# Optimization experiments

Hardware: AMD Instinct MI355X
Metric: run time of the kernel (lower is better)

The kernel has to match this reference:

```python
import jax, jax.numpy as jnp
import numpy as np

DT = 0.01        # base_dt from __init__
DT_SCALE = 1.0   # forward default


def setup_inputs() -> dict:
    key = jax.random.key(0)
    k1, k2, k3, k4, k5 = jax.random.split(key, 5)
    B, D, R = 4096, 512, 128
    x = jax.random.normal(k1, (B, D), dtype=jnp.float32)
    v = jax.random.normal(k2, (B, D), dtype=jnp.float32)
    force = jax.random.normal(k3, (B, D), dtype=jnp.float32)
    U = jax.random.normal(k4, (D, R), dtype=jnp.float32) * (1.0 / np.sqrt(D))
    W = jax.random.normal(k5, (R, D), dtype=jnp.float32) * (1.0 / np.sqrt(R))
    return {"x": x, "v": v, "force": force, "U": U, "W": W, "steps": 8}


def reference(x, v, force, U, W, steps):
    dt = DT * DT_SCALE
    # Dormand-Prince (DP5) tableau
    a21 = 1/5
    a31, a32 = 3/40, 9/40
    a41, a42, a43 = 44/45, -56/15, 32/9
    a51, a52, a53, a54 = 19372/6561, -25360/2187, 64448/6561, -212/729
    a61, a62, a63, a64, a65 = 9017/3168, -355/33, 46732/5247, 49/176, -5103/18656
    b1, b3, b4, b5, b6 = 35/384, 500/1113, 125/192, -2187/6784, 11/84

    def dynamics(tx, tv):
        # low-rank Christoffel: gamma(v, x) = ((v @ U) * (x @ U)) @ W
        acc = -jnp.einsum('br,rd->bd', (tv @ U) * (tx @ U), W)
        return acc + force

    def step(carry, _):
        cx, cv = carry
        k1x = cv
        k1v = dynamics(cx, cv)
        x2 = cx + dt * (a21 * k1x); v2 = cv + dt * (a21 * k1v)
        k2x = v2; k2v = dynamics(x2, v2)
        x3 = cx + dt * (a31 * k1x + a32 * k2x)
        v3 = cv + dt * (a31 * k1v + a32 * k2v)
        k3x = v3; k3v = dynamics(x3, v3)
        x4 = cx + dt * (a41 * k1x + a42 * k2x + a43 * k3x)
        v4 = cv + dt * (a41 * k1v + a42 * k2v + a43 * k3v)
        k4x = v4; k4v = dynamics(x4, v4)
        x5 = cx + dt * (a51 * k1x + a52 * k2x + a53 * k3x + a54 * k4x)
        v5 = cv + dt * (a51 * k1v + a52 * k2v + a53 * k3v + a54 * k4v)
        k5x = v5; k5v = dynamics(x5, v5)
        x6 = cx + dt * (a61 * k1x + a62 * k2x + a63 * k3x + a64 * k4x + a65 * k5x)
        v6 = cv + dt * (a61 * k1v + a62 * k2v + a63 * k3v + a64 * k4v + a65 * k5v)
        k6x = v6; k6v = dynamics(x6, v6)
        nx = cx + dt * (b1 * k1x + b3 * k3x + b4 * k4x + b5 * k5x + b6 * k6x)
        nv = cv + dt * (b1 * k1v + b3 * k3v + b4 * k4v + b5 * k5v + b6 * k6v)
        return (nx, nv), None

    (fx, fv), _ = jax.lax.scan(step, (x, v), None, length=steps)
    return fx, fv
```

## Files before the change

kernel.cpp:

```cpp
#include <hip/hip_runtime.h>


typedef _Float16 v8h __attribute__((ext_vector_type(8)));
typedef float v4f __attribute__((ext_vector_type(4)));
typedef unsigned short u16;
typedef unsigned int u32;

#define MFMAH __builtin_amdgcn_mfma_f32_16x16x32_f16
#define INV2048 4.8828125e-4f
#define INV256  0.00390625f
#define SSTR 144

__device__ __forceinline__ float swap8(float x){
  return __int_as_float(
    __builtin_amdgcn_mov_dpp(__float_as_int(x), 0x128, 0xf, 0xf, true));
}

struct Tab {
  double a[7][7]; double b[7]; double A[7]; double XC[7][7]; double XF[7]; double cxc[7];
};
static constexpr Tab make_tab() {
  Tab t{};
  t.a[2][1]=1.0/5;
  t.a[3][1]=3.0/40;       t.a[3][2]=9.0/40;
  t.a[4][1]=44.0/45;      t.a[4][2]=-56.0/15;      t.a[4][3]=32.0/9;
  t.a[5][1]=19372.0/6561; t.a[5][2]=-25360.0/2187; t.a[5][3]=64448.0/6561; t.a[5][4]=-212.0/729;
  t.a[6][1]=9017.0/3168;  t.a[6][2]=-355.0/33;     t.a[6][3]=46732.0/5247; t.a[6][4]=49.0/176; t.a[6][5]=-5103.0/18656;
  t.b[1]=35.0/384; t.b[2]=0.0; t.b[3]=500.0/1113; t.b[4]=125.0/192; t.b[5]=-2187.0/6784; t.b[6]=11.0/84;
  for (int i=1;i<=6;++i){ double s=0; for(int j=1;j<i;++j) s+=t.a[i][j]; t.A[i]=s; }
  for (int i=1;i<=6;++i) for(int l=1;l<i;++l){ double s=0; for(int j=l+1;j<i;++j) s+=t.a[i][j]*t.a[j][l]; t.XC[i][l]=s; }
  for (int i=1;i<=6;++i){ double s=0; for(int j=1;j<i;++j) s+=t.a[i][j]*t.A[j]; t.XF[i]=s; }
  for (int j=1;j<=6;++j){ double s=0; for (int i=j+1;i<=6;++i) s+=t.b[i]*t.a[i][j]; t.cxc[j]=s; }
  return t;
}
static constexpr Tab TB = make_tab();

__device__ __forceinline__ int decode_steps(const void* p){
  int v = *(const int*)p;
  if (v >= 1 && v <= 512) return v;
  float f = *(const float*)p;
  if (f >= 1.f && f <= 512.f) return (int)f;
  return 8;
}
__device__ __forceinline__ void split2s(float x, _Float16& h, _Float16& l){
  h = (_Float16)x;
  l = (_Float16)((x - (float)h) * 2048.0f);
}

#define WS_GH 0
#define WS_GL 16384
#define WS_UH 32768
#define WS_UL 98304
#define WS_WH 163840
#define WS_WL 229376

__global__ __launch_bounds__(512) void k_prep(const float* __restrict__ Ug,
                                              const float* __restrict__ Wg,
                                              _Float16* __restrict__ ws){
  const int tid = threadIdx.x;
  if (blockIdx.x >= 8) {
    int t = (blockIdx.x - 8)*512 + tid;
    if (t < 65536) {
      int r = t >> 7, c = t & 127;
      _Float16 h, l; split2s(Ug[t]*256.f, h, l);
      int kb=r>>5, q2=(r>>3)&3, j=r&7, n2=c>>4, cl=c&15;
      int slot = ((n2*16+kb)*64 + q2*16+cl)*8 + j;
      ws[WS_UH + slot] = h; ws[WS_UL + slot] = l;
    } else {
      int idx = t - 65536;
      int r = idx >> 9, c = idx & 511;
      _Float16 h, l; split2s(Wg[idx]*256.f, h, l);
      int kb=r>>5, q2=(r>>3)&3, j=r&7, n2=c>>4, cl=c&15;
      int slot = ((n2*4+kb)*64 + q2*16+cl)*8 + j;
      ws[WS_WH + slot] = h; ws[WS_WL + slot] = l;
    }
  } else {
    const int b = blockIdx.x;
    const int ww = tid >> 6, lane = tid & 63, q = lane >> 4, c16 = lane & 15;
    const int nb = ww;
    v4f aH = {0,0,0,0}, aC0 = {0,0,0,0}, aC1 = {0,0,0,0};
    #pragma unroll
    for (int kb = 0; kb < 16; ++kb) {
      const float* wp = Wg + (b*16 + c16)*512 + kb*32 + q*8;
      float4 w0 = *(const float4*)wp;
      float4 w1 = *(const float4*)(wp + 4);
      float wv[8] = {w0.x,w0.y,w0.z,w0.w, w1.x,w1.y,w1.z,w1.w};
      v8h Ah, Al, Bh, Bl;
      #pragma unroll
      for (int j = 0; j < 8; ++j) {
        _Float16 h, l; split2s(-wv[j], h, l);
        Ah[j] = h; Al[j] = l;
        float uv = Ug[(kb*32 + q*8 + j)*128 + nb*16 + c16] * 256.f;
        split2s(uv, h, l);
        Bh[j] = h; Bl[j] = l;
      }
      aH = MFMAH(Ah, Bh, aH, 0,0,0);
      if (kb & 1) {
        aC1 = MFMAH(Ah, Bl, aC1, 0,0,0);
        aC1 = MFMAH(Al, Bh, aC1, 0,0,0);
      } else {
        aC0 = MFMAH(Ah, Bl, aC0, 0,0,0);
        aC0 = MFMAH(Al, Bh, aC0, 0,0,0);
      }
    }
    #pragma unroll
    for (int r = 0; r < 4; ++r) {
      float g = aH[r] + (aC0[r] + aC1[r])*INV2048;
      _Float16 h, l; split2s(g, h, l);
      int m = b*16 + 4*q + r, n = nb*16 + c16;
      int slot = (((n>>4)*4 + (m>>5))*64 + ((m>>3)&3)*16 + (n&15))*8 + (m&7);
      ws[WS_GH + slot] = h; ws[WS_GL + slot] = l;
    }
  }
}

#define ARENA 49920

__global__ __launch_bounds__(512,4) void dp5_main(
    const float* __restrict__ xg, const float* __restrict__ vg,
    const float* __restrict__ fg, const void* stepsp,
    const _Float16* __restrict__ ws, float* __restrict__ outg)
{
  __shared__ __align__(16) char arena[ARENA];
  _Float16* base = (_Float16*)arena;
  const _Float16* uH = ws + WS_UH;
  const _Float16* uL = ws + WS_UL;
  const _Float16* wH = ws + WS_WH;
  const _Float16* wL = ws + WS_WL;

  const int tid  = threadIdx.x;
  const int ww   = tid >> 6;
  const int lane = tid & 63;
  const int q    = lane >> 4;
  const int c16  = lane & 15;
  const int nb   = ww;
  const int kcol = nb*16 + c16;
  const int srcl = (q>>1)*16 + c16;
  const bool odd = (q & 1);
  const int rb   = blockIdx.x * 8;
  const int S    = decode_steps(stepsp);
  const float dt = 0.01f;
  const int  brow = c16 & 7;
  const bool hiC  = (c16 >= 8);
  const int  kc0  = nb*16 + 4*q + (hiC ? 2 : 0);

  v8h Gh[4], Gl[4];
  #pragma unroll
  for (int kb = 0; kb < 4; ++kb) {
    int off = ((nb*4 + kb)*64 + lane)*8;
    Gh[kb] = *(const v8h*)(ws + WS_GH + off);
    Gl[kb] = *(const v8h*)(ws + WS_GL + off);
  }

  _Float16* tH = base;
  _Float16* tL = base + 12480;
  const int r16 = tid >> 5, c0 = (tid & 31)*16;
  float xU0[2], vU0[2], fU0[2];
  {
    {
      const float* sp = (r16 < 8) ? (xg + (rb + r16)*512) : (vg + (rb + r16 - 8)*512);
      sp += c0;
      float4 g0 = *(const float4*)(sp);
      float4 g1 = *(const float4*)(sp + 4);
      float4 g2 = *(const float4*)(sp + 8);
      float4 g3 = *(const float4*)(sp + 12);
      float vals[16] = {g0.x,g0.y,g0.z,g0.w, g1.x,g1.y,g1.z,g1.w,
                        g2.x,g2.y,g2.z,g2.w, g3.x,g3.y,g3.z,g3.w};
      v8h vh0, vh1, vl0, vl1;
      #pragma unroll
      for (int j = 0; j < 8; ++j) {
        _Float16 h, l;
        split2s(vals[j], h, l);     vh0[j] = h; vl0[j] = l;
        split2s(vals[8+j], h, l);   vh1[j] = h; vl1[j] = l;
      }
      int o = r16*520 + c0;
      *(v8h*)(tH + o) = vh0; *(v8h*)(tH + o + 8) = vh1;
      *(v8h*)(tL + o) = vl0; *(v8h*)(tL + o + 8) = vl1;
    }
    if (r16 < 8) {
      const float* sp = fg + (rb + r16)*512 + c0;
      float4 g0 = *(const float4*)(sp);
      float4 g1 = *(const float4*)(sp + 4);
      float4 g2 = *(const float4*)(sp + 8);
      float4 g3 = *(const float4*)(sp + 12);
      float vals[16] = {g0.x,g0.y,g0.z,g0.w, g1.x,g1.y,g1.z,g1.w,
                        g2.x,g2.y,g2.z,g2.w, g3.x,g3.y,g3.z,g3.w};
      v8h vh0, vh1, vl0, vl1;
      #pragma unroll
      for (int j = 0; j < 8; ++j) {
        _Float16 h, l;
        split2s(vals[j], h, l);     vh0[j] = h; vl0[j] = l;
        split2s(vals[8+j], h, l);   vh1[j] = h; vl1[j] = l;
      }
      int o = (16 + r16)*520 + c0;
      *(v8h*)(tH + o) = vh0; *(v8h*)(tH + o + 8) = vh1;
      *(v8h*)(tL + o) = vl0; *(v8h*)(tL + o + 8) = vl1;
    }
    __syncthreads();

    v4f aH0={0,0,0,0}, aH1={0,0,0,0}, aC0={0,0,0,0}, aC1={0,0,0,0};
    v4f bH0={0,0,0,0}, bH1={0,0,0,0}, bC0={0,0,0,0}, bC1={0,0,0,0};
    const int arow1 = (c16 < 8) ? (16 + c16) : c16;
    #pragma unroll
    for (int kb = 0; kb < 16; ++kb) {
      int ao0 = c16*520 + kb*32 + q*8;
      int ao1 = arow1*520 + kb*32 + q*8;
      v8h Ah0 = *(const v8h*)(tH + ao0);
      v8h Al0 = *(const v8h*)(tL + ao0);
      v8h Ah1 = *(const v8h*)(tH + ao1);
      v8h Al1 = *(const v8h*)(tL + ao1);
      int bo = ((nb*16 + kb)*64 + lane)*8;
      v8h Bh = *(const v8h*)(uH + bo);
      v8h Bl = *(const v8h*)(uL + bo);
      if (kb & 1) {
        aH1 = MFMAH(Ah0, Bh, aH1, 0,0,0);
        aC1 = MFMAH(Ah0, Bl, aC1, 0,0,0);
        aC1 = MFMAH(Al0, Bh, aC1, 0,0,0);
        bH1 = MFMAH(Ah1, Bh, bH1, 0,0,0);
        bC1 = MFMAH(Ah1, Bl, bC1, 0,0,0);
        bC1 = MFMAH(Al1, Bh, bC1, 0,0,0);
      } else {
        aH0 = MFMAH(Ah0, Bh, aH0, 0,0,0);
        aC0 = MFMAH(Ah0, Bl, aC0, 0,0,0);
        aC0 = MFMAH(Al0, Bh, aC0, 0,0,0);
        bH0 = MFMAH(Ah1, Bh, bH0, 0,0,0);
        bC0 = MFMAH(Ah1, Bl, bC0, 0,0,0);
        bC0 = MFMAH(Al1, Bh, bC0, 0,0,0);
      }
    }
    float at0 = ((aH0[0]+aH1[0]) + (aC0[0]+aC1[0])*INV2048)*INV256;
    float at1 = ((aH0[1]+aH1[1]) + (aC0[1]+aC1[1])*INV2048)*INV256;
    float at2 = ((aH0[2]+aH1[2]) + (aC0[2]+aC1[2])*INV2048)*INV256;
    float at3 = ((aH0[3]+aH1[3]) + (aC0[3]+aC1[3])*INV2048)*INV256;
    float bt0 = ((bH0[0]+bH1[0]) + (bC0[0]+bC1[0])*INV2048)*INV256;
    float bt1 = ((bH0[1]+bH1[1]) + (bC0[1]+bC1[1])*INV2048)*INV256;
    float bt2 = ((bH0[2]+bH1[2]) + (bC0[2]+bC1[2])*INV2048)*INV256;
    float bt3 = ((bH0[3]+bH1[3]) + (bC0[3]+bC1[3])*INV2048)*INV256;
    {
      float sx0=__shfl(at0,srcl,64), sx1=__shfl(at1,srcl,64);
      float sx2=__shfl(at2,srcl,64), sx3=__shfl(at3,srcl,64);
      xU0[0] = odd ? sx2 : sx0; xU0[1] = odd ? sx3 : sx1;
      int srclv = srcl + 32;
      float sv0=__shfl(at0,srclv,64), sv1=__shfl(at1,srclv,64);
      float sv2=__shfl(at2,srclv,64), sv3=__shfl(at3,srclv,64);
      vU0[0] = odd ? sv2 : sv0; vU0[1] = odd ? sv3 : sv1;
    }
    {
      float sf0=__shfl(bt0,srcl,64), sf1=__shfl(bt1,srcl,64);
      float sf2=__shfl(bt2,srcl,64), sf3=__shfl(bt3,srcl,64);
      fU0[0] = odd ? sf2 : sf0; fU0[1] = odd ? sf3 : sf1;
    }
    __syncthreads();
  }

  float cxU2[2], cvU2[2], fU2[2];
  {
    float* T = (float*)arena;
    #pragma unroll
    for (int p2 = 0; p2 < 3; ++p2) {
      float i0 = (p2==0) ? xU0[0] : (p2==1) ? vU0[0] : fU0[0];
      float i1 = (p2==0) ? xU0[1] : (p2==1) ? vU0[1] : fU0[1];
      T[(2*q + 0)*132 + kcol] = i0;
      T[(2*q + 1)*132 + kcol] = i1;
      __syncthreads();
      float2 t2 = *(const float2*)(T + brow*132 + kc0);
      float* o = (p2==0) ? cxU2 : (p2==1) ? cvU2 : fU2;
      o[0] = t2.x; o[1] = t2.y;
      __syncthreads();
    }
  }

  float kU6[6][2], Rr2[2], QXa2[2];
  #pragma unroll
  for (int j = 0; j < 2; ++j) {
    Rr2[j] = 0.f; QXa2[j] = 0.f;
    #pragma unroll
    for (int l = 0; l < 6; ++l) kU6[l][j] = 0.f;
  }

  int pb = 0;
  for (int s = 0; s < S; ++s) {
    float accX[2], accV[2], Pbs[2], Pxcs[2];
    #pragma unroll
    for (int j = 0; j < 2; ++j) { accX[j]=0.f; accV[j]=0.f; Pbs[j]=0.f; Pxcs[j]=0.f; }

    #pragma unroll
    for (int i = 1; i <= 6; ++i) {
      _Float16* bT = base + (pb ? 2304 : 0);
      const float dtA   = dt*(float)TB.A[i];
      const float dt2XF = dt*dt*(float)TB.XF[i];
      const float bi    = (float)TB.b[i];
      const float ci    = (float)TB.cxc[i];
      {
        union { _Float16 h[2]; u32 u; } ph, pl;
        #pragma unroll
        for (int j2 = 0; j2 < 2; ++j2) {
          float vv = cvU2[j2] + dtA*fU2[j2];
          float xx = cxU2[j2] + dtA*cvU2[j2] + dt2XF*fU2[j2];
          #pragma unroll
          for (int l = 1; l < i; ++l) {
            vv += (dt*(float)TB.a[i][l]) * kU6[l-1][j2];
            xx += (dt*dt*(float)TB.XC[i][l]) * kU6[l-1][j2];
          }
          float p = vv*xx;
          Pbs[j2] += bi*p; Pxcs[j2] += ci*p;
          _Float16 h, l2; split2s(p, h, l2);
          ph.h[j2] = h; pl.h[j2] = l2;
        }
        *(u32*)(bT + brow*SSTR + kc0)       = ph.u;
        *(u32*)(bT + (8+brow)*SSTR + kc0)   = pl.u;
      }
      __syncthreads();
      const _Float16* bp = bT + c16*SSTR + q*8;
      v8h B0 = *(const v8h*)(bp);
      v8h B1 = *(const v8h*)(bp + 32);
      v8h B2 = *(const v8h*)(bp + 64);
      v8h B3 = *(const v8h*)(bp + 96);
      v4f C1 = {0,0,0,0}, C2 = {0,0,0,0};
      C1 = MFMAH(Gh[0], B0, C1, 0,0,0);  C2 = MFMAH(Gl[0], B0, C2, 0,0,0);
      C1 = MFMAH(Gh[1], B1, C1, 0,0,0);  C2 = MFMAH(Gl[1], B1, C2, 0,0,0);
      C1 = MFMAH(Gh[2], B2, C1, 0,0,0);  C2 = MFMAH(Gl[2], B2, C2, 0,0,0);
      C1 = MFMAH(Gh[3], B3, C1, 0,0,0);  C2 = MFMAH(Gl[3], B3, C2, 0,0,0);
      float kv[4];
      #pragma unroll
      for (int r = 0; r < 4; ++r) {
        float oth = swap8(C1[r]);
        kv[r] = (C1[r] + (oth + C2[r])*INV2048)*INV256;
      }
      float k2 = swap8(kv[2]);
      float k3 = swap8(kv[3]);
      float kva = hiC ? k2 : kv[0];
      float kvb = hiC ? k3 : kv[1];
      kU6[i-1][0] = kva; kU6[i-1][1] = kvb;
      accX[0] += ci*kva; accV[0] += bi*kva;
      accX[1] += ci*kvb; accV[1] += bi*kvb;
      pb ^= 1;
    }

    #pragma unroll
    for (int j = 0; j < 2; ++j) {
      float nx = cxU2[j] + dt*cvU2[j] + dt*dt*(accX[j] + 0.5f*fU2[j]);
      cvU2[j] += dt*(accV[j] + fU2[j]);
      cxU2[j]  = nx;
      QXa2[j] += Rr2[j] + Pxcs[j];
      Rr2[j]  += Pbs[j];
    }
  }

  __syncthreads();
  _Float16* RQh = base;
  _Float16* RQl = base + 2176;
  {
    union { _Float16 h[2]; u32 u; } t1, t2, t3, t4;
    #pragma unroll
    for (int j2 = 0; j2 < 2; ++j2) {
      _Float16 h, l;
      split2s(Rr2[j2], h, l);  t1.h[j2] = h; t2.h[j2] = l;
      split2s(QXa2[j2], h, l); t3.h[j2] = h; t4.h[j2] = l;
    }
    *(u32*)(RQh + brow*136 + kc0)     = t1.u;
    *(u32*)(RQl + brow*136 + kc0)     = t2.u;
    *(u32*)(RQh + (8+brow)*136 + kc0) = t3.u;
    *(u32*)(RQl + (8+brow)*136 + kc0) = t4.u;
  }
  __syncthreads();

  float* axs = (float*)(arena + 9216);
  float* abs_ = (float*)(arena + 25600);

  #pragma unroll
  for (int cbi = 0; cbi < 4; ++cbi) {
    int cb = nb*4 + cbi;
    v4f aH={0,0,0,0}, aC0={0,0,0,0}, aC1={0,0,0,0};
    #pragma unroll
    for (int kb = 0; kb < 4; ++kb) {
      int bo = ((cb*4 + kb)*64 + lane)*8;
      v8h Bh = *(const v8h*)(wH + bo);
      v8h Bl = *(const v8h*)(wL + bo);
      int ao = c16*136 + kb*32 + q*8;
      v8h Ah = *(const v8h*)(RQh + ao);
      v8h Al = *(const v8h*)(RQl + ao);
      aH = MFMAH(Ah, Bh, aH, 0,0,0);
      if (kb & 1) {
        aC1 = MFMAH(Ah, Bl, aC1, 0,0,0);
        aC1 = MFMAH(Al, Bh, aC1, 0,0,0);
      } else {
        aC0 = MFMAH(Ah, Bl, aC0, 0,0,0);
        aC0 = MFMAH(Al, Bh, aC0, 0,0,0);
      }
    }
    float r0 = (aH[0] + (aC0[0]+aC1[0])*INV2048)*INV256;
    float r1 = (aH[1] + (aC0[1]+aC1[1])*INV2048)*INV256;
    float r2 = (aH[2] + (aC0[2]+aC1[2])*INV2048)*INV256;
    float r3 = (aH[3] + (aC0[3]+aC1[3])*INV2048)*INV256;
    float o0 = __shfl_xor(r0, 32, 64);
    float o1 = __shfl_xor(r1, 32, 64);
    float o2 = __shfl_xor(r2, 32, 64);
    float o3 = __shfl_xor(r3, 32, 64);
    if (q < 2) {
      float abv[4] = {r0, r1, r2, r3};
      float axv[4] = {o0, o1, o2, o3};
      #pragma unroll
      for (int i4 = 0; i4 < 4; ++i4) {
        int lrow = 4*q + i4;
        int lcol = cb*16 + c16;
        axs[lrow*512 + lcol]  = axv[i4];
        abs_[lrow*512 + lcol] = abv[i4];
      }
    }
  }
  __syncthreads();

  const float Sdt = (float)S * dt;
  #pragma unroll
  for (int half = 0; half < 2; ++half) {
    int flat = half*2048 + tid*4;
    int row  = flat >> 9;
    int col  = flat & 511;
    int go   = (rb + row)*512 + col;
    float4 xv = *(const float4*)(xg + go);
    float4 vv = *(const float4*)(vg + go);
    float4 fv = *(const float4*)(fg + go);
    float4 axf = *(const float4*)(axs + flat);
    float4 abf = *(const float4*)(abs_ + flat);
    float4 o1, o2;
    o1.x = xv.x + Sdt*vv.x + 0.5f*Sdt*Sdt*fv.x - dt*dt*axf.x;
    o1.y = xv.y + Sdt*vv.y + 0.5f*Sdt*Sdt*fv.y - dt*dt*axf.y;
    o1.z = xv.z + Sdt*vv.z + 0.5f*Sdt*Sdt*fv.z - dt*dt*axf.z;
    o1.w = xv.w + Sdt*vv.w + 0.5f*Sdt*Sdt*fv.w - dt*dt*axf.w;
    o2.x = vv.x + Sdt*fv.x - dt*abf.x;
    o2.y = vv.y + Sdt*fv.y - dt*abf.y;
    o2.z = vv.z + Sdt*fv.z - dt*abf.z;
    o2.w = vv.w + Sdt*fv.w - dt*abf.w;
    *(float4*)(outg + go) = o1;
    *(float4*)(outg + 2097152 + go) = o2;
  }
}

extern "C" void kernel_launch(void* const* d_in, const int* in_sizes, int n_in,
                              void* d_out, int out_size, void* d_ws, size_t ws_size,
                              hipStream_t stream) {
  const float* x = (const float*)d_in[0];
  const float* v = (const float*)d_in[1];
  const float* f = (const float*)d_in[2];
  const float* U = (const float*)d_in[3];
  const float* W = (const float*)d_in[4];
  _Float16* ws = (_Float16*)d_ws;

  k_prep<<<dim3(264), dim3(512), 0, stream>>>(U, W, ws);
  dp5_main<<<dim3(512), dim3(512), 0, stream>>>(
      x, v, f, d_in[5], ws, (float*)d_out);
}
```

Baseline: 136.4 us.

## Precompute next-stage RK partial sums off critical path, trim post-MFMA swaps, stagger block start

Before each stage's barrier and MFMA, the code now precomputes the partial sums for the next stage's inputs from the already-known k values. Only the newest k term is added after the MFMA result arrives, which shortens the serial dependency chain between stages. The post-MFMA reduction is reordered so the DPP swaps run on raw accumulator values and the selects happen before the arithmetic, using fewer dependent swaps. It also adds an s_sleep for blocks with blockIdx bit 8 set, staggering their start, which can shift contention but also adds idle time.

```diff
diff --git a/kernel.cpp b/kernel.cpp
--- a/kernel.cpp
+++ b/kernel.cpp
@@ -127,6 +127,8 @@
   const _Float16* uL = ws + WS_UL;
   const _Float16* wH = ws + WS_WH;
   const _Float16* wL = ws + WS_WL;
+
+  if (blockIdx.x & 256) __builtin_amdgcn_s_sleep(19);
 
   const int tid  = threadIdx.x;
   const int ww   = tid >> 6;
@@ -284,23 +286,27 @@
     #pragma unroll
     for (int j = 0; j < 2; ++j) { accX[j]=0.f; accV[j]=0.f; Pbs[j]=0.f; Pxcs[j]=0.f; }
 
+    float vvP[2], xxP[2];
+    #pragma unroll
+    for (int j2 = 0; j2 < 2; ++j2) {
+      vvP[j2] = cvU2[j2] + (dt*(float)TB.A[1])*fU2[j2];
+      xxP[j2] = cxU2[j2] + (dt*(float)TB.A[1])*cvU2[j2] + (dt*dt*(float)TB.XF[1])*fU2[j2];
+    }
+
     #pragma unroll
     for (int i = 1; i <= 6; ++i) {
       _Float16* bT = base + (pb ? 2304 : 0);
-      const float dtA   = dt*(float)TB.A[i];
-      const float dt2XF = dt*dt*(float)TB.XF[i];
       const float bi    = (float)TB.b[i];
       const float ci    = (float)TB.cxc[i];
       {
         union { _Float16 h[2]; u32 u; } ph, pl;
         #pragma unroll
         for (int j2 = 0; j2 < 2; ++j2) {
-          float vv = cvU2[j2] + dtA*fU2[j2];
-          float xx = cxU2[j2] + dtA*cvU2[j2] + dt2XF*fU2[j2];
-          #pragma unroll
-          for (int l = 1; l < i; ++l) {
-            vv += (dt*(float)TB.a[i][l]) * kU6[l-1][j2];
-            xx += (dt*dt*(float)TB.XC[i][l]) * kU6[l-1][j2];
+          float vv = vvP[j2];
+          float xx = xxP[j2];
+          if (i >= 2) {
+            vv += (dt*(float)TB.a[i][i-1]) * kU6[i-2][j2];
+            xx += (dt*dt*(float)TB.XC[i][i-1]) * kU6[i-2][j2];
           }
           float p = vv*xx;
           Pbs[j2] += bi*p; Pxcs[j2] += ci*p;
@@ -309,6 +315,19 @@
         }
         *(u32*)(bT + brow*SSTR + kc0)       = ph.u;
         *(u32*)(bT + (8+brow)*SSTR + kc0)   = pl.u;
+      }
+      if (i < 6) {
+        #pragma unroll
+        for (int j2 = 0; j2 < 2; ++j2) {
+          float vv = cvU2[j2] + (dt*(float)TB.A[i+1])*fU2[j2];
+          float xx = cxU2[j2] + (dt*(float)TB.A[i+1])*cvU2[j2] + (dt*dt*(float)TB.XF[i+1])*fU2[j2];
+          #pragma unroll
+          for (int l = 1; l < i; ++l) {
+            vv += (dt*(float)TB.a[i+1][l]) * kU6[l-1][j2];
+            xx += (dt*dt*(float)TB.XC[i+1][l]) * kU6[l-1][j2];
+          }
+          vvP[j2] = vv; xxP[j2] = xx;
+        }
       }
       __syncthreads();
       const _Float16* bp = bT + c16*SSTR + q*8;
@@ -321,19 +340,21 @@
       C1 = MFMAH(Gh[1], B1, C1, 0,0,0);  C2 = MFMAH(Gl[1], B1, C2, 0,0,0);
       C1 = MFMAH(Gh[2], B2, C1, 0,0,0);  C2 = MFMAH(Gl[2], B2, C2, 0,0,0);
       C1 = MFMAH(Gh[3], B3, C1, 0,0,0);  C2 = MFMAH(Gl[3], B3, C2, 0,0,0);
-      float kv[4];
-      #pragma unroll
-      for (int r = 0; r < 4; ++r) {
-        float oth = swap8(C1[r]);
-        kv[r] = (C1[r] + (oth + C2[r])*INV2048)*INV256;
-      }
-      float k2 = swap8(kv[2]);
-      float k3 = swap8(kv[3]);
-      float kva = hiC ? k2 : kv[0];
-      float kvb = hiC ? k3 : kv[1];
-      kU6[i-1][0] = kva; kU6[i-1][1] = kvb;
-      accX[0] += ci*kva; accV[0] += bi*kva;
-      accX[1] += ci*kvb; accV[1] += bi*kvb;
+      {
+        float sa0 = swap8(C1[0]), sa2 = swap8(C1[2]), sc2 = swap8(C2[2]);
+        float sb1 = swap8(C1[1]), sb3 = swap8(C1[3]), sd3 = swap8(C2[3]);
+        float m_a = hiC ? sa2   : C1[0];
+        float n_a = hiC ? C1[2] : sa0;
+        float c_a = hiC ? sc2   : C2[0];
+        float m_b = hiC ? sb3   : C1[1];
+        float n_b = hiC ? C1[3] : sb1;
+        float c_b = hiC ? sd3   : C2[1];
+        float kva = (m_a + (n_a + c_a)*INV2048)*INV256;
+        float kvb = (m_b + (n_b + c_b)*INV2048)*INV256;
+        kU6[i-1][0] = kva; kU6[i-1][1] = kvb;
+        accX[0] += ci*kva; accV[0] += bi*kva;
+        accX[1] += ci*kvb; accV[1] += bi*kvb;
+      }
       pb ^= 1;
     }
 
```

After: 136.2 us (median of 2 runs). No clear change (-0.2%).

## Halve block size to 256 threads with two column groups per wave

Applied to the files above, without the earlier changes.

Restructures the main DP5 kernel to use 4 waves per block instead of 8, with each wave handling two 16-column groups of the rank dimension. Per-wave register state doubles (kU, accumulators, G fragments, MFMA accumulators) and the epilogue keeps the A operand fragments in registers across column blocks. The prologue now transposes all three projections with a single LDS round trip instead of three, and the upper half of the blocks issue an s_sleep at the start to stagger their launch. The aim is fewer threads per barrier and less redundant LDS traffic, at the cost of higher register pressure and less occupancy per block.

```diff
diff --git a/kernel.cpp b/kernel.cpp
--- a/kernel.cpp
+++ b/kernel.cpp
@@ -3,8 +3,8 @@
 
 typedef _Float16 v8h __attribute__((ext_vector_type(8)));
 typedef float v4f __attribute__((ext_vector_type(4)));
-typedef unsigned short u16;
 typedef unsigned int u32;
+typedef unsigned long long u64;
 
 #define MFMAH __builtin_amdgcn_mfma_f32_16x16x32_f16
 #define INV2048 4.8828125e-4f
@@ -116,7 +116,7 @@
 
 #define ARENA 49920
 
-__global__ __launch_bounds__(512,4) void dp5_main(
+__global__ __launch_bounds__(256,2) void dp5_main(
     const float* __restrict__ xg, const float* __restrict__ vg,
     const float* __restrict__ fg, const void* stepsp,
     const _Float16* __restrict__ ws, float* __restrict__ outg)
@@ -128,78 +128,66 @@
   const _Float16* wH = ws + WS_WH;
   const _Float16* wL = ws + WS_WL;
 
+  if (blockIdx.x & 256) __builtin_amdgcn_s_sleep(19);
+
   const int tid  = threadIdx.x;
-  const int ww   = tid >> 6;
+  const int w    = tid >> 6;
   const int lane = tid & 63;
   const int q    = lane >> 4;
   const int c16  = lane & 15;
-  const int nb   = ww;
-  const int kcol = nb*16 + c16;
-  const int srcl = (q>>1)*16 + c16;
-  const bool odd = (q & 1);
   const int rb   = blockIdx.x * 8;
   const int S    = decode_steps(stepsp);
   const float dt = 0.01f;
   const int  brow = c16 & 7;
   const bool hiC  = (c16 >= 8);
-  const int  kc0  = nb*16 + 4*q + (hiC ? 2 : 0);
-
-  v8h Gh[4], Gl[4];
-  #pragma unroll
-  for (int kb = 0; kb < 4; ++kb) {
-    int off = ((nb*4 + kb)*64 + lane)*8;
-    Gh[kb] = *(const v8h*)(ws + WS_GH + off);
-    Gl[kb] = *(const v8h*)(ws + WS_GL + off);
-  }
+  const int  kc0n = w*32 + (hiC ? 16 : 0) + 4*q;
 
   _Float16* tH = base;
   _Float16* tL = base + 12480;
-  const int r16 = tid >> 5, c0 = (tid & 31)*16;
-  float xU0[2], vU0[2], fU0[2];
   {
+    const int row = tid >> 4;
+    const int c0  = (tid & 15) * 32;
     {
-      const float* sp = (r16 < 8) ? (xg + (rb + r16)*512) : (vg + (rb + r16 - 8)*512);
+      const float* sp = (row < 8) ? (xg + (rb + row)*512) : (vg + (rb + row - 8)*512);
       sp += c0;
-      float4 g0 = *(const float4*)(sp);
-      float4 g1 = *(const float4*)(sp + 4);
-      float4 g2 = *(const float4*)(sp + 8);
-      float4 g3 = *(const float4*)(sp + 12);
-      float vals[16] = {g0.x,g0.y,g0.z,g0.w, g1.x,g1.y,g1.z,g1.w,
-                        g2.x,g2.y,g2.z,g2.w, g3.x,g3.y,g3.z,g3.w};
-      v8h vh0, vh1, vl0, vl1;
-      #pragma unroll
-      for (int j = 0; j < 8; ++j) {
-        _Float16 h, l;
-        split2s(vals[j], h, l);     vh0[j] = h; vl0[j] = l;
-        split2s(vals[8+j], h, l);   vh1[j] = h; vl1[j] = l;
-      }
-      int o = r16*520 + c0;
-      *(v8h*)(tH + o) = vh0; *(v8h*)(tH + o + 8) = vh1;
-      *(v8h*)(tL + o) = vl0; *(v8h*)(tL + o + 8) = vl1;
-    }
-    if (r16 < 8) {
-      const float* sp = fg + (rb + r16)*512 + c0;
-      float4 g0 = *(const float4*)(sp);
-      float4 g1 = *(const float4*)(sp + 4);
-      float4 g2 = *(const float4*)(sp + 8);
-      float4 g3 = *(const float4*)(sp + 12);
-      float vals[16] = {g0.x,g0.y,g0.z,g0.w, g1.x,g1.y,g1.z,g1.w,
-                        g2.x,g2.y,g2.z,g2.w, g3.x,g3.y,g3.z,g3.w};
-      v8h vh0, vh1, vl0, vl1;
-      #pragma unroll
-      for (int j = 0; j < 8; ++j) {
-        _Float16 h, l;
-        split2s(vals[j], h, l);     vh0[j] = h; vl0[j] = l;
-        split2s(vals[8+j], h, l);   vh1[j] = h; vl1[j] = l;
-      }
-      int o = (16 + r16)*520 + c0;
-      *(v8h*)(tH + o) = vh0; *(v8h*)(tH + o + 8) = vh1;
-      *(v8h*)(tL + o) = vl0; *(v8h*)(tL + o + 8) = vl1;
-    }
-    __syncthreads();
-
-    v4f aH0={0,0,0,0}, aH1={0,0,0,0}, aC0={0,0,0,0}, aC1={0,0,0,0};
-    v4f bH0={0,0,0,0}, bH1={0,0,0,0}, bC0={0,0,0,0}, bC1={0,0,0,0};
+      #pragma unroll
+      for (int b2 = 0; b2 < 4; ++b2) {
+        float4 g0 = *(const float4*)(sp + b2*8);
+        float4 g1 = *(const float4*)(sp + b2*8 + 4);
+        float vals[8] = {g0.x,g0.y,g0.z,g0.w, g1.x,g1.y,g1.z,g1.w};
+        v8h vh, vl;
+        #pragma unroll
+        for (int j = 0; j < 8; ++j) { _Float16 h,l; split2s(vals[j],h,l); vh[j]=h; vl[j]=l; }
+        int o = row*520 + c0 + b2*8;
+        *(v8h*)(tH + o) = vh; *(v8h*)(tL + o) = vl;
+      }
+    }
+    if (tid < 128) {
+      const int rowf = tid >> 4;
+      const float* sp = fg + (rb + rowf)*512 + c0;
+      #pragma unroll
+      for (int b2 = 0; b2 < 4; ++b2) {
+        float4 g0 = *(const float4*)(sp + b2*8);
+        float4 g1 = *(const float4*)(sp + b2*8 + 4);
+        float vals[8] = {g0.x,g0.y,g0.z,g0.w, g1.x,g1.y,g1.z,g1.w};
+        v8h vh, vl;
+        #pragma unroll
+        for (int j = 0; j < 8; ++j) { _Float16 h,l; split2s(vals[j],h,l); vh[j]=h; vl[j]=l; }
+        int o = (16 + rowf)*520 + c0 + b2*8;
+        *(v8h*)(tH + o) = vh; *(v8h*)(tL + o) = vl;
+      }
+    }
+  }
+  __syncthreads();
+
+  float cxU4[4], cvU4[4], fU4[4];
+  {
+    v4f AH0[2],AH1[2],AC0[2],AC1[2],BH0[2],BH1[2],BC0[2],BC1[2];
+    #pragma unroll
+    for (int g=0; g<2; ++g){
+      AH0[g]=v4f{0,0,0,0}; AH1[g]=v4f{0,0,0,0}; AC0[g]=v4f{0,0,0,0}; AC1[g]=v4f{0,0,0,0};
+      BH0[g]=v4f{0,0,0,0}; BH1[g]=v4f{0,0,0,0}; BC0[g]=v4f{0,0,0,0}; BC1[g]=v4f{0,0,0,0};
+    }
     const int arow1 = (c16 < 8) ? (16 + c16) : c16;
     #pragma unroll
     for (int kb = 0; kb < 16; ++kb) {
@@ -209,80 +197,85 @@
       v8h Al0 = *(const v8h*)(tL + ao0);
       v8h Ah1 = *(const v8h*)(tH + ao1);
       v8h Al1 = *(const v8h*)(tL + ao1);
-      int bo = ((nb*16 + kb)*64 + lane)*8;
-      v8h Bh = *(const v8h*)(uH + bo);
-      v8h Bl = *(const v8h*)(uL + bo);
-      if (kb & 1) {
-        aH1 = MFMAH(Ah0, Bh, aH1, 0,0,0);
-        aC1 = MFMAH(Ah0, Bl, aC1, 0,0,0);
-        aC1 = MFMAH(Al0, Bh, aC1, 0,0,0);
-        bH1 = MFMAH(Ah1, Bh, bH1, 0,0,0);
-        bC1 = MFMAH(Ah1, Bl, bC1, 0,0,0);
-        bC1 = MFMAH(Al1, Bh, bC1, 0,0,0);
+      #pragma unroll
+      for (int g = 0; g < 2; ++g) {
+        int bo = (((2*w+g)*16 + kb)*64 + lane)*8;
+        v8h Bh = *(const v8h*)(uH + bo);
+        v8h Bl = *(const v8h*)(uL + bo);
+        if (kb & 1) {
+          AH1[g] = MFMAH(Ah0, Bh, AH1[g], 0,0,0);
+          AC1[g] = MFMAH(Ah0, Bl, AC1[g], 0,0,0);
+          AC1[g] = MFMAH(Al0, Bh, AC1[g], 0,0,0);
+          BH1[g] = MFMAH(Ah1, Bh, BH1[g], 0,0,0);
+          BC1[g] = MFMAH(Ah1, Bl, BC1[g], 0,0,0);
+          BC1[g] = MFMAH(Al1, Bh, BC1[g], 0,0,0);
+        } else {
+          AH0[g] = MFMAH(Ah0, Bh, AH0[g], 0,0,0);
+          AC0[g] = MFMAH(Ah0, Bl, AC0[g], 0,0,0);
+          AC0[g] = MFMAH(Al0, Bh, AC0[g], 0,0,0);
+          BH0[g] = MFMAH(Ah1, Bh, BH0[g], 0,0,0);
+          BC0[g] = MFMAH(Ah1, Bl, BC0[g], 0,0,0);
+          BC0[g] = MFMAH(Al1, Bh, BC0[g], 0,0,0);
+        }
+      }
+    }
+    __syncthreads();
+    float* T = (float*)arena;
+    #pragma unroll
+    for (int g = 0; g < 2; ++g) {
+      float ar[4], br[4];
+      #pragma unroll
+      for (int r = 0; r < 4; ++r) {
+        ar[r] = ((AH0[g][r]+AH1[g][r]) + (AC0[g][r]+AC1[g][r])*INV2048)*INV256;
+        br[r] = ((BH0[g][r]+BH1[g][r]) + (BC0[g][r]+BC1[g][r])*INV2048)*INV256;
+      }
+      int colc = (2*w+g)*16 + c16;
+      if (q < 2) {
+        #pragma unroll
+        for (int r = 0; r < 4; ++r) {
+          T[(4*q+r)*132 + colc]        = ar[r];
+          T[2112 + (4*q+r)*132 + colc] = br[r];
+        }
       } else {
-        aH0 = MFMAH(Ah0, Bh, aH0, 0,0,0);
-        aC0 = MFMAH(Ah0, Bl, aC0, 0,0,0);
-        aC0 = MFMAH(Al0, Bh, aC0, 0,0,0);
-        bH0 = MFMAH(Ah1, Bh, bH0, 0,0,0);
-        bC0 = MFMAH(Ah1, Bl, bC0, 0,0,0);
-        bC0 = MFMAH(Al1, Bh, bC0, 0,0,0);
-      }
-    }
-    float at0 = ((aH0[0]+aH1[0]) + (aC0[0]+aC1[0])*INV2048)*INV256;
-    float at1 = ((aH0[1]+aH1[1]) + (aC0[1]+aC1[1])*INV2048)*INV256;
-    float at2 = ((aH0[2]+aH1[2]) + (aC0[2]+aC1[2])*INV2048)*INV256;
-    float at3 = ((aH0[3]+aH1[3]) + (aC0[3]+aC1[3])*INV2048)*INV256;
-    float bt0 = ((bH0[0]+bH1[0]) + (bC0[0]+bC1[0])*INV2048)*INV256;
-    float bt1 = ((bH0[1]+bH1[1]) + (bC0[1]+bC1[1])*INV2048)*INV256;
-    float bt2 = ((bH0[2]+bH1[2]) + (bC0[2]+bC1[2])*INV2048)*INV256;
-    float bt3 = ((bH0[3]+bH1[3]) + (bC0[3]+bC1[3])*INV2048)*INV256;
-    {
-      float sx0=__shfl(at0,srcl,64), sx1=__shfl(at1,srcl,64);
-      float sx2=__shfl(at2,srcl,64), sx3=__shfl(at3,srcl,64);
-      xU0[0] = odd ? sx2 : sx0; xU0[1] = odd ? sx3 : sx1;
-      int srclv = srcl + 32;
-      float sv0=__shfl(at0,srclv,64), sv1=__shfl(at1,srclv,64);
-      float sv2=__shfl(at2,srclv,64), sv3=__shfl(at3,srclv,64);
-      vU0[0] = odd ? sv2 : sv0; vU0[1] = odd ? sv3 : sv1;
-    }
-    {
-      float sf0=__shfl(bt0,srcl,64), sf1=__shfl(bt1,srcl,64);
-      float sf2=__shfl(bt2,srcl,64), sf3=__shfl(bt3,srcl,64);
-      fU0[0] = odd ? sf2 : sf0; fU0[1] = odd ? sf3 : sf1;
+        #pragma unroll
+        for (int r = 0; r < 4; ++r) {
+          T[1056 + (4*(q-2)+r)*132 + colc] = ar[r];
+        }
+      }
     }
     __syncthreads();
-  }
-
-  float cxU2[2], cvU2[2], fU2[2];
-  {
-    float* T = (float*)arena;
-    #pragma unroll
-    for (int p2 = 0; p2 < 3; ++p2) {
-      float i0 = (p2==0) ? xU0[0] : (p2==1) ? vU0[0] : fU0[0];
-      float i1 = (p2==0) ? xU0[1] : (p2==1) ? vU0[1] : fU0[1];
-      T[(2*q + 0)*132 + kcol] = i0;
-      T[(2*q + 1)*132 + kcol] = i1;
-      __syncthreads();
-      float2 t2 = *(const float2*)(T + brow*132 + kc0);
-      float* o = (p2==0) ? cxU2 : (p2==1) ? cvU2 : fU2;
-      o[0] = t2.x; o[1] = t2.y;
-      __syncthreads();
-    }
-  }
-
-  float kU6[6][2], Rr2[2], QXa2[2];
+    float4 tx = *(const float4*)(T +        brow*132 + kc0n);
+    float4 tv = *(const float4*)(T + 1056 + brow*132 + kc0n);
+    float4 tf = *(const float4*)(T + 2112 + brow*132 + kc0n);
+    cxU4[0]=tx.x; cxU4[1]=tx.y; cxU4[2]=tx.z; cxU4[3]=tx.w;
+    cvU4[0]=tv.x; cvU4[1]=tv.y; cvU4[2]=tv.z; cvU4[3]=tv.w;
+    fU4[0]=tf.x;  fU4[1]=tf.y;  fU4[2]=tf.z;  fU4[3]=tf.w;
+    __syncthreads();
+  }
+
+  v8h Gh[2][4], Gl[2][4];
   #pragma unroll
-  for (int j = 0; j < 2; ++j) {
-    Rr2[j] = 0.f; QXa2[j] = 0.f;
-    #pragma unroll
-    for (int l = 0; l < 6; ++l) kU6[l][j] = 0.f;
+  for (int g = 0; g < 2; ++g)
+    #pragma unroll
+    for (int kb = 0; kb < 4; ++kb) {
+      int off = (((2*w+g)*4 + kb)*64 + lane)*8;
+      Gh[g][kb] = *(const v8h*)(ws + WS_GH + off);
+      Gl[g][kb] = *(const v8h*)(ws + WS_GL + off);
+    }
+
+  float kU[6][4], Rr[4], QX[4];
+  #pragma unroll
+  for (int j = 0; j < 4; ++j) {
+    Rr[j] = 0.f; QX[j] = 0.f;
+    #pragma unroll
+    for (int l = 0; l < 6; ++l) kU[l][j] = 0.f;
   }
 
   int pb = 0;
   for (int s = 0; s < S; ++s) {
-    float accX[2], accV[2], Pbs[2], Pxcs[2];
-    #pragma unroll
-    for (int j = 0; j < 2; ++j) { accX[j]=0.f; accV[j]=0.f; Pbs[j]=0.f; Pxcs[j]=0.f; }
+    float accX[4], accV[4], Pb[4], Pxc[4];
+    #pragma unroll
+    for (int j = 0; j < 4; ++j) { accX[j]=0.f; accV[j]=0.f; Pb[j]=0.f; Pxc[j]=0.f; }
 
     #pragma unroll
     for (int i = 1; i <= 6; ++i) {
@@ -292,23 +285,23 @@
       const float bi    = (float)TB.b[i];
       const float ci    = (float)TB.cxc[i];
       {
-        union { _Float16 h[2]; u32 u; } ph, pl;
-        #pragma unroll
-        for (int j2 = 0; j2 < 2; ++j2) {
-          float vv = cvU2[j2] + dtA*fU2[j2];
-          float xx = cxU2[j2] + dtA*cvU2[j2] + dt2XF*fU2[j2];
+        union { _Float16 h[4]; u64 u; } ph, pl;
+        #pragma unroll
+        for (int j2 = 0; j2 < 4; ++j2) {
+          float vv = cvU4[j2] + dtA*fU4[j2];
+          float xx = cxU4[j2] + dtA*cvU4[j2] + dt2XF*fU4[j2];
           #pragma unroll
           for (int l = 1; l < i; ++l) {
-            vv += (dt*(float)TB.a[i][l]) * kU6[l-1][j2];
-            xx += (dt*dt*(float)TB.XC[i][l]) * kU6[l-1][j2];
+            vv += (dt*(float)TB.a[i][l]) * kU[l-1][j2];
+            xx += (dt*dt*(float)TB.XC[i][l]) * kU[l-1][j2];
           }
           float p = vv*xx;
-          Pbs[j2] += bi*p; Pxcs[j2] += ci*p;
+          Pb[j2] += bi*p; Pxc[j2] += ci*p;
           _Float16 h, l2; split2s(p, h, l2);
           ph.h[j2] = h; pl.h[j2] = l2;
         }
-        *(u32*)(bT + brow*SSTR + kc0)       = ph.u;
-        *(u32*)(bT + (8+brow)*SSTR + kc0)   = pl.u;
+        *(u64*)(bT + brow*SSTR + kc0n)     = ph.u;
+        *(u64*)(bT + (8+brow)*SSTR + kc0n) = pl.u;
       }
       __syncthreads();
       const _Float16* bp = bT + c16*SSTR + q*8;
@@ -316,34 +309,34 @@
       v8h B1 = *(const v8h*)(bp + 32);
       v8h B2 = *(const v8h*)(bp + 64);
       v8h B3 = *(const v8h*)(bp + 96);
-      v4f C1 = {0,0,0,0}, C2 = {0,0,0,0};
-      C1 = MFMAH(Gh[0], B0, C1, 0,0,0);  C2 = MFMAH(Gl[0], B0, C2, 0,0,0);
-      C1 = MFMAH(Gh[1], B1, C1, 0,0,0);  C2 = MFMAH(Gl[1], B1, C2, 0,0,0);
-      C1 = MFMAH(Gh[2], B2, C1, 0,0,0);  C2 = MFMAH(Gl[2], B2, C2, 0,0,0);
-      C1 = MFMAH(Gh[3], B3, C1, 0,0,0);  C2 = MFMAH(Gl[3], B3, C2, 0,0,0);
-      float kv[4];
+      v4f C1[2], C2[2];
+      #pragma unroll
+      for (int g = 0; g < 2; ++g) {
+        C1[g] = v4f{0,0,0,0}; C2[g] = v4f{0,0,0,0};
+        C1[g] = MFMAH(Gh[g][0], B0, C1[g], 0,0,0);  C2[g] = MFMAH(Gl[g][0], B0, C2[g], 0,0,0);
+        C1[g] = MFMAH(Gh[g][1], B1, C1[g], 0,0,0);  C2[g] = MFMAH(Gl[g][1], B1, C2[g], 0,0,0);
+        C1[g] = MFMAH(Gh[g][2], B2, C1[g], 0,0,0);  C2[g] = MFMAH(Gl[g][2], B2, C2[g], 0,0,0);
+        C1[g] = MFMAH(Gh[g][3], B3, C1[g], 0,0,0);  C2[g] = MFMAH(Gl[g][3], B3, C2[g], 0,0,0);
+      }
       #pragma unroll
       for (int r = 0; r < 4; ++r) {
-        float oth = swap8(C1[r]);
-        kv[r] = (C1[r] + (oth + C2[r])*INV2048)*INV256;
-      }
-      float k2 = swap8(kv[2]);
-      float k3 = swap8(kv[3]);
-      float kva = hiC ? k2 : kv[0];
-      float kvb = hiC ? k3 : kv[1];
-      kU6[i-1][0] = kva; kU6[i-1][1] = kvb;
-      accX[0] += ci*kva; accV[0] += bi*kva;
-      accX[1] += ci*kvb; accV[1] += bi*kvb;
+        float kv0 = (C1[0][r] + (swap8(C1[0][r]) + C2[0][r])*INV2048)*INV256;
+        float kv1 = (C1[1][r] + (swap8(C1[1][r]) + C2[1][r])*INV2048)*INV256;
+        float sk1 = swap8(kv1);
+        float kk  = hiC ? sk1 : kv0;
+        kU[i-1][r] = kk;
+        accX[r] += ci*kk; accV[r] += bi*kk;
+      }
       pb ^= 1;
     }
 
     #pragma unroll
-    for (int j = 0; j < 2; ++j) {
-      float nx = cxU2[j] + dt*cvU2[j] + dt*dt*(accX[j] + 0.5f*fU2[j]);
-      cvU2[j] += dt*(accV[j] + fU2[j]);
-      cxU2[j]  = nx;
-      QXa2[j] += Rr2[j] + Pxcs[j];
-      Rr2[j]  += Pbs[j];
+    for (int j = 0; j < 4; ++j) {
+      float nx = cxU4[j] + dt*cvU4[j] + dt*dt*(accX[j] + 0.5f*fU4[j]);
+      cvU4[j] += dt*(accV[j] + fU4[j]);
+      cxU4[j]  = nx;
+      QX[j] += Rr[j] + Pxc[j];
+      Rr[j] += Pb[j];
     }
   }
 
@@ -351,61 +344,69 @@
   _Float16* RQh = base;
   _Float16* RQl = base + 2176;
   {
-    union { _Float16 h[2]; u32 u; } t1, t2, t3, t4;
-    #pragma unroll
-    for (int j2 = 0; j2 < 2; ++j2) {
+    union { _Float16 h[4]; u64 u; } t1, t2, t3, t4;
+    #pragma unroll
+    for (int j2 = 0; j2 < 4; ++j2) {
       _Float16 h, l;
-      split2s(Rr2[j2], h, l);  t1.h[j2] = h; t2.h[j2] = l;
-      split2s(QXa2[j2], h, l); t3.h[j2] = h; t4.h[j2] = l;
-    }
-    *(u32*)(RQh + brow*136 + kc0)     = t1.u;
-    *(u32*)(RQl + brow*136 + kc0)     = t2.u;
-    *(u32*)(RQh + (8+brow)*136 + kc0) = t3.u;
-    *(u32*)(RQl + (8+brow)*136 + kc0) = t4.u;
+      split2s(Rr[j2], h, l);  t1.h[j2] = h; t2.h[j2] = l;
+      split2s(QX[j2], h, l);  t3.h[j2] = h; t4.h[j2] = l;
+    }
+    *(u64*)(RQh + brow*136 + kc0n)     = t1.u;
+    *(u64*)(RQl + brow*136 + kc0n)     = t2.u;
+    *(u64*)(RQh + (8+brow)*136 + kc0n) = t3.u;
+    *(u64*)(RQl + (8+brow)*136 + kc0n) = t4.u;
   }
   __syncthreads();
 
-  float* axs = (float*)(arena + 9216);
+  v8h EAh[4], EAl[4];
+  #pragma unroll
+  for (int kb = 0; kb < 4; ++kb) {
+    int ao = c16*136 + kb*32 + q*8;
+    EAh[kb] = *(const v8h*)(RQh + ao);
+    EAl[kb] = *(const v8h*)(RQl + ao);
+  }
+
+  float* axs  = (float*)(arena + 9216);
   float* abs_ = (float*)(arena + 25600);
 
   #pragma unroll
-  for (int cbi = 0; cbi < 4; ++cbi) {
-    int cb = nb*4 + cbi;
-    v4f aH={0,0,0,0}, aC0={0,0,0,0}, aC1={0,0,0,0};
-    #pragma unroll
-    for (int kb = 0; kb < 4; ++kb) {
-      int bo = ((cb*4 + kb)*64 + lane)*8;
-      v8h Bh = *(const v8h*)(wH + bo);
-      v8h Bl = *(const v8h*)(wL + bo);
-      int ao = c16*136 + kb*32 + q*8;
-      v8h Ah = *(const v8h*)(RQh + ao);
-      v8h Al = *(const v8h*)(RQl + ao);
-      aH = MFMAH(Ah, Bh, aH, 0,0,0);
-      if (kb & 1) {
-        aC1 = MFMAH(Ah, Bl, aC1, 0,0,0);
-        aC1 = MFMAH(Al, Bh, aC1, 0,0,0);
-      } else {
-        aC0 = MFMAH(Ah, Bl, aC0, 0,0,0);
-        aC0 = MFMAH(Al, Bh, aC0, 0,0,0);
-      }
-    }
-    float r0 = (aH[0] + (aC0[0]+aC1[0])*INV2048)*INV256;
-    float r1 = (aH[1] + (aC0[1]+aC1[1])*INV2048)*INV256;
-    float r2 = (aH[2] + (aC0[2]+aC1[2])*INV2048)*INV256;
-    float r3 = (aH[3] + (aC0[3]+aC1[3])*INV2048)*INV256;
-    float o0 = __shfl_xor(r0, 32, 64);
-    float o1 = __shfl_xor(r1, 32, 64);
-    float o2 = __shfl_xor(r2, 32, 64);
-    float o3 = __shfl_xor(r3, 32, 64);
-    if (q < 2) {
-      float abv[4] = {r0, r1, r2, r3};
-      float axv[4] = {o0, o1, o2, o3};
-      #pragma unroll
-      for (int i4 = 0; i4 < 4; ++i4) {
-        int lrow = 4*q + i4;
-        int lcol = cb*16 + c16;
-        axs[lrow*512 + lcol]  = axv[i4];
-        abs_[lrow*512 + lcol] = abv[i4];
+  for (int g = 0; g < 2; ++g) {
+    #pragma unroll
+    for (int cbi = 0; cbi < 4; ++cbi) {
+      int cb = (2*w+g)*4 + cbi;
+      v4f aH={0,0,0,0}, aC0={0,0,0,0}, aC1={0,0,0,0};
+      #pragma unroll
+      for (int kb = 0; kb < 4; ++kb) {
+        int bo = ((cb*4 + kb)*64 + lane)*8;
+        v8h Bh = *(const v8h*)(wH + bo);
+        v8h Bl = *(const v8h*)(wL + bo);
+        aH = MFMAH(EAh[kb], Bh, aH, 0,0,0);
+        if (kb & 1) {
+          aC1 = MFMAH(EAh[kb], Bl, aC1, 0,0,0);
+          aC1 = MFMAH(EAl[kb], Bh, aC1, 0,0,0);
+        } else {
+          aC0 = MFMAH(EAh[kb], Bl, aC0, 0,0,0);
+          aC0 = MFMAH(EAl[kb], Bh, aC0, 0,0,0);
+        }
+      }
+      float r0 = (aH[0] + (aC0[0]+aC1[0])*INV2048)*INV256;
+      float r1 = (aH[1] + (aC0[1]+aC1[1])*INV2048)*INV256;
+      float r2 = (aH[2] + (aC0[2]+aC1[2])*INV2048)*INV256;
+      float r3 = (aH[3] + (aC0[3]+aC1[3])*INV2048)*INV256;
+      float o0 = __shfl_xor(r0, 32, 64);
+      float o1 = __shfl_xor(r1, 32, 64);
+      float o2 = __shfl_xor(r2, 32, 64);
+      float o3 = __shfl_xor(r3, 32, 64);
+      if (q < 2) {
+        float abv[4] = {r0, r1, r2, r3};
+        float axv[4] = {o0, o1, o2, o3};
+        #pragma unroll
+        for (int i4 = 0; i4 < 4; ++i4) {
+          int lrow = 4*q + i4;
+          int lcol = cb*16 + c16;
+          axs[lrow*512 + lcol]  = axv[i4];
+          abs_[lrow*512 + lcol] = abv[i4];
+        }
       }
     }
   }
@@ -413,8 +414,8 @@
 
   const float Sdt = (float)S * dt;
   #pragma unroll
-  for (int half = 0; half < 2; ++half) {
-    int flat = half*2048 + tid*4;
+  for (int half = 0; half < 4; ++half) {
+    int flat = half*1024 + tid*4;
     int row  = flat >> 9;
     int col  = flat & 511;
     int go   = (rb + row)*512 + col;
@@ -448,6 +449,6 @@
   _Float16* ws = (_Float16*)d_ws;
 
   k_prep<<<dim3(264), dim3(512), 0, stream>>>(U, W, ws);
-  dp5_main<<<dim3(512), dim3(512), 0, stream>>>(
+  dp5_main<<<dim3(512), dim3(256), 0, stream>>>(
       x, v, f, d_in[5], ws, (float*)d_out);
 }
```

New measurement: 142.1 us. 1.04x slower.
